# Performance work log

Measured on AMD Instinct MI355X. Metric: run time of the kernel, lower is better.

## Reference

```python
import jax, jax.numpy as jnp
import numpy as np

PATCH = 8
NP_H = 1024 // PATCH  # 128
NP_W = 1024 // PATCH  # 128
HID = (8, 8, 8)
IN_DIM = 2


def setup_inputs() -> dict:
    key = jax.random.key(0)
    ks = jax.random.split(key, 5)
    light_direction = jax.random.normal(ks[0], (32, IN_DIM), dtype=jnp.float32)
    w1 = jax.random.normal(ks[1], (NP_H, NP_W, HID[0], IN_DIM), dtype=jnp.float32) * 0.01
    b1 = jnp.zeros((NP_H, NP_W, HID[0]), dtype=jnp.float32)
    w2 = jax.random.normal(ks[2], (NP_H, NP_W, HID[1], HID[0]), dtype=jnp.float32) * 0.01
    b2 = jnp.zeros((NP_H, NP_W, HID[1]), dtype=jnp.float32)
    w3 = jax.random.normal(ks[3], (NP_H, NP_W, HID[2], HID[1]), dtype=jnp.float32) * 0.01
    b3 = jnp.zeros((NP_H, NP_W, HID[2]), dtype=jnp.float32)
    w_out = jax.random.normal(ks[4], (NP_H, NP_W, 3, HID[2]), dtype=jnp.float32) * 0.01
    b_out = jnp.zeros((NP_H, NP_W, 3), dtype=jnp.float32)
    return {"light_direction": light_direction, "w1": w1, "b1": b1,
            "w2": w2, "b2": b2, "w3": w3, "b3": b3,
            "w_out": w_out, "b_out": b_out}


def reference(light_direction, w1, b1, w2, b2, w3, b3, w_out, b_out):
    B = light_direction.shape[0]
    # broadcast light dir to every patch: [B, H, W, in_dim]
    x = jnp.broadcast_to(light_direction[:, None, None, :], (B, NP_H, NP_W, IN_DIM))
    # per-patch tiny MLP: einsum over input dim (batched tiny GEMV per patch)
    h = jax.nn.relu(jnp.einsum('bhwi,hwoi->bhwo', x, w1) + b1)
    h = jax.nn.relu(jnp.einsum('bhwi,hwoi->bhwo', h, w2) + b2)
    h = jax.nn.relu(jnp.einsum('bhwi,hwoi->bhwo', h, w3) + b3)
    out = jax.nn.sigmoid(jnp.einsum('bhwi,hwoi->bhwo', h, w_out) + b_out)  # [B,H,W,3]
    # tile each patch value to patch_size x patch_size pixels -> [B,1024,1024,3]
    out = jnp.broadcast_to(out[:, :, None, :, None, :],
                           (B, NP_H, PATCH, NP_W, PATCH, 3))
    return out.reshape(B, NP_H * PATCH, NP_W * PATCH, 3)
```

## Files before the change

### kernel.cpp

```cpp
#include <hip/hip_runtime.h>
#include <math.h>

#define NP 128
#define NB 32

typedef float vf4 __attribute__((ext_vector_type(4)));

__global__ __launch_bounds__(256) void fused_relight(
    const float* __restrict__ ld,
    const float* __restrict__ w1,
    const float* __restrict__ b1,
    const float* __restrict__ w2,
    const float* __restrict__ b2,
    const float* __restrict__ w3,
    const float* __restrict__ b3,
    const float* __restrict__ wo,
    const float* __restrict__ bo,
    float* __restrict__ out)
{
    int bid = blockIdx.x;
    int ph = bid >> 5;
    int b  = bid & 31;
    int t  = threadIdx.x;

    __shared__ float cl[NP * 3];

    if (t < NP) {
        int p = ph * NP + t;
        float x0 = ld[2 * b + 0];
        float x1 = ld[2 * b + 1];

        float h[8], g[8];
        {
            const float* W  = w1 + (size_t)p * 16;
            const float* Bv = b1 + (size_t)p * 8;
#pragma unroll
            for (int o = 0; o < 8; ++o) {
                float s = fmaf(W[2 * o + 0], x0, fmaf(W[2 * o + 1], x1, Bv[o]));
                h[o] = fmaxf(0.f, s);
            }
        }
        {
            const float* W  = w2 + (size_t)p * 64;
            const float* Bv = b2 + (size_t)p * 8;
#pragma unroll
            for (int o = 0; o < 8; ++o) {
                float s = Bv[o];
#pragma unroll
                for (int i = 0; i < 8; ++i) s = fmaf(W[8 * o + i], h[i], s);
                g[o] = fmaxf(0.f, s);
            }
        }
        {
            const float* W  = w3 + (size_t)p * 64;
            const float* Bv = b3 + (size_t)p * 8;
#pragma unroll
            for (int o = 0; o < 8; ++o) {
                float s = Bv[o];
#pragma unroll
                for (int i = 0; i < 8; ++i) s = fmaf(W[8 * o + i], g[i], s);
                h[o] = fmaxf(0.f, s);
            }
        }
        {
            const float* W  = wo + (size_t)p * 24;
            const float* Bv = bo + (size_t)p * 3;
#pragma unroll
            for (int c = 0; c < 3; ++c) {
                float s = Bv[c];
#pragma unroll
                for (int i = 0; i < 8; ++i) s = fmaf(W[8 * c + i], h[i], s);
                cl[t * 3 + c] = 1.f / (1.f + expf(-s));
            }
        }
    }
    __syncthreads();

    vf4* op = (vf4*)out + (size_t)b * 786432 + (size_t)ph * 6144;

#pragma unroll
    for (int k = 0; k < 24; ++k) {
        int c  = k * 256 + t;
        int row = c / 768;
        int ct = c - row * 768;
        int pw = ct / 6;
        int s  = ct % 3;

        float c0 = cl[pw * 3 + 0];
        float c1 = cl[pw * 3 + 1];
        float c2 = cl[pw * 3 + 2];
        float ca = (s == 0) ? c0 : ((s == 1) ? c1 : c2);
        float cb = (s == 0) ? c1 : ((s == 1) ? c2 : c0);
        float cc = (s == 0) ? c2 : ((s == 1) ? c0 : c1);

        vf4 v;
        v.x = ca; v.y = cb; v.z = cc; v.w = ca;
        __builtin_nontemporal_store(v, &op[c]);
    }
}

extern "C" void kernel_launch(void* const* d_in, const int* in_sizes, int n_in,
                              void* d_out, int out_size, void* d_ws, size_t ws_size,
                              hipStream_t stream) {
    const float* ld = (const float*)d_in[0];
    const float* w1 = (const float*)d_in[1];
    const float* b1 = (const float*)d_in[2];
    const float* w2 = (const float*)d_in[3];
    const float* b2 = (const float*)d_in[4];
    const float* w3 = (const float*)d_in[5];
    const float* b3 = (const float*)d_in[6];
    const float* wo = (const float*)d_in[7];
    const float* bo = (const float*)d_in[8];

    float* out = (float*)d_out;

    fused_relight<<<dim3(NP * NB), dim3(256), 0, stream>>>(
        ld, w1, b1, w2, b2, w3, b3, wo, bo, out);
}
```

Before: 95.79 us.

## Split fused kernel into full-occupancy MLP pass and separate tile-write pass

Splits the work into two kernels. The first runs the per-patch MLP on every thread and writes colors to a workspace buffer. The second loads those colors into shared memory and does the broadcast tile writes. This removes the idle half-block during MLP compute and the serialization of compute before stores within each block, at the cost of an extra launch and a round trip of about 6 MB through the workspace. The old fused kernel remains as a fallback when the workspace is too small.

```diff
diff --git a/kernel.cpp b/kernel.cpp
--- a/kernel.cpp
+++ b/kernel.cpp
@@ -6,7 +6,7 @@
 
 typedef float vf4 __attribute__((ext_vector_type(4)));
 
-__global__ __launch_bounds__(256) void fused_relight(
+__global__ __launch_bounds__(256) void mlp_colors(
     const float* __restrict__ ld,
     const float* __restrict__ w1,
     const float* __restrict__ b1,
@@ -16,67 +16,76 @@
     const float* __restrict__ b3,
     const float* __restrict__ wo,
     const float* __restrict__ bo,
+    float* __restrict__ color)
+{
+    unsigned int tid = blockIdx.x * blockDim.x + threadIdx.x;
+    int p = tid & 16383;
+    int b = tid >> 14;
+
+    float x0 = ld[2 * b + 0];
+    float x1 = ld[2 * b + 1];
+
+    float h[8], g[8];
+    {
+        const float* W  = w1 + (size_t)p * 16;
+        const float* Bv = b1 + (size_t)p * 8;
+#pragma unroll
+        for (int o = 0; o < 8; ++o) {
+            float s = fmaf(W[2 * o + 0], x0, fmaf(W[2 * o + 1], x1, Bv[o]));
+            h[o] = fmaxf(0.f, s);
+        }
+    }
+    {
+        const float* W  = w2 + (size_t)p * 64;
+        const float* Bv = b2 + (size_t)p * 8;
+#pragma unroll
+        for (int o = 0; o < 8; ++o) {
+            float s = Bv[o];
+#pragma unroll
+            for (int i = 0; i < 8; ++i) s = fmaf(W[8 * o + i], h[i], s);
+            g[o] = fmaxf(0.f, s);
+        }
+    }
+    {
+        const float* W  = w3 + (size_t)p * 64;
+        const float* Bv = b3 + (size_t)p * 8;
+#pragma unroll
+        for (int o = 0; o < 8; ++o) {
+            float s = Bv[o];
+#pragma unroll
+            for (int i = 0; i < 8; ++i) s = fmaf(W[8 * o + i], g[i], s);
+            h[o] = fmaxf(0.f, s);
+        }
+    }
+    {
+        const float* W  = wo + (size_t)p * 24;
+        const float* Bv = bo + (size_t)p * 3;
+        float* cp = color + ((size_t)b * 16384 + (size_t)p) * 3;
+#pragma unroll
+        for (int c = 0; c < 3; ++c) {
+            float s = Bv[c];
+#pragma unroll
+            for (int i = 0; i < 8; ++i) s = fmaf(W[8 * c + i], h[i], s);
+            cp[c] = 1.f / (1.f + expf(-s));
+        }
+    }
+}
+
+__global__ __launch_bounds__(256) void tile_write_f32(
+    const float* __restrict__ color,
     float* __restrict__ out)
 {
     int bid = blockIdx.x;
-    int ph = bid >> 5;
-    int b  = bid & 31;
-    int t  = threadIdx.x;
+    int t = threadIdx.x;
 
     __shared__ float cl[NP * 3];
 
-    if (t < NP) {
-        int p = ph * NP + t;
-        float x0 = ld[2 * b + 0];
-        float x1 = ld[2 * b + 1];
-
-        float h[8], g[8];
-        {
-            const float* W  = w1 + (size_t)p * 16;
-            const float* Bv = b1 + (size_t)p * 8;
-#pragma unroll
-            for (int o = 0; o < 8; ++o) {
-                float s = fmaf(W[2 * o + 0], x0, fmaf(W[2 * o + 1], x1, Bv[o]));
-                h[o] = fmaxf(0.f, s);
-            }
-        }
-        {
-            const float* W  = w2 + (size_t)p * 64;
-            const float* Bv = b2 + (size_t)p * 8;
-#pragma unroll
-            for (int o = 0; o < 8; ++o) {
-                float s = Bv[o];
-#pragma unroll
-                for (int i = 0; i < 8; ++i) s = fmaf(W[8 * o + i], h[i], s);
-                g[o] = fmaxf(0.f, s);
-            }
-        }
-        {
-            const float* W  = w3 + (size_t)p * 64;
-            const float* Bv = b3 + (size_t)p * 8;
-#pragma unroll
-            for (int o = 0; o < 8; ++o) {
-                float s = Bv[o];
-#pragma unroll
-                for (int i = 0; i < 8; ++i) s = fmaf(W[8 * o + i], g[i], s);
-                h[o] = fmaxf(0.f, s);
-            }
-        }
-        {
-            const float* W  = wo + (size_t)p * 24;
-            const float* Bv = bo + (size_t)p * 3;
-#pragma unroll
-            for (int c = 0; c < 3; ++c) {
-                float s = Bv[c];
-#pragma unroll
-                for (int i = 0; i < 8; ++i) s = fmaf(W[8 * c + i], h[i], s);
-                cl[t * 3 + c] = 1.f / (1.f + expf(-s));
-            }
-        }
-    }
+    const float* src = color + (size_t)bid * (NP * 3);
+    cl[t] = src[t >= 384 ? 0 : t];
+    if (t < 128) cl[256 + t] = src[256 + t];
     __syncthreads();
 
-    vf4* op = (vf4*)out + (size_t)b * 786432 + (size_t)ph * 6144;
+    vf4* op = (vf4*)out + (size_t)bid * 6144;
 
 #pragma unroll
     for (int k = 0; k < 24; ++k) {
@@ -95,6 +104,87 @@
 
         vf4 v;
         v.x = ca; v.y = cb; v.z = cc; v.w = ca;
+        __builtin_nontemporal_store(v, &op[c]);
+    }
+}
+
+__global__ __launch_bounds__(256) void fused_relight(
+    const float* __restrict__ ld, const float* __restrict__ w1,
+    const float* __restrict__ b1, const float* __restrict__ w2,
+    const float* __restrict__ b2, const float* __restrict__ w3,
+    const float* __restrict__ b3, const float* __restrict__ wo,
+    const float* __restrict__ bo, float* __restrict__ out)
+{
+    int bid = blockIdx.x;
+    int ph = bid >> 5;
+    int b  = bid & 31;
+    int t  = threadIdx.x;
+
+    __shared__ float cl[NP * 3];
+
+    if (t < NP) {
+        int p = ph * NP + t;
+        float x0 = ld[2 * b + 0];
+        float x1 = ld[2 * b + 1];
+        float h[8], g[8];
+        {
+            const float* W  = w1 + (size_t)p * 16;
+            const float* Bv = b1 + (size_t)p * 8;
+#pragma unroll
+            for (int o = 0; o < 8; ++o)
+                h[o] = fmaxf(0.f, fmaf(W[2*o], x0, fmaf(W[2*o+1], x1, Bv[o])));
+        }
+        {
+            const float* W  = w2 + (size_t)p * 64;
+            const float* Bv = b2 + (size_t)p * 8;
+#pragma unroll
+            for (int o = 0; o < 8; ++o) {
+                float s = Bv[o];
+#pragma unroll
+                for (int i = 0; i < 8; ++i) s = fmaf(W[8*o+i], h[i], s);
+                g[o] = fmaxf(0.f, s);
+            }
+        }
+        {
+            const float* W  = w3 + (size_t)p * 64;
+            const float* Bv = b3 + (size_t)p * 8;
+#pragma unroll
+            for (int o = 0; o < 8; ++o) {
+                float s = Bv[o];
+#pragma unroll
+                for (int i = 0; i < 8; ++i) s = fmaf(W[8*o+i], g[i], s);
+                h[o] = fmaxf(0.f, s);
+            }
+        }
+        {
+            const float* W  = wo + (size_t)p * 24;
+            const float* Bv = bo + (size_t)p * 3;
+#pragma unroll
+            for (int c = 0; c < 3; ++c) {
+                float s = Bv[c];
+#pragma unroll
+                for (int i = 0; i < 8; ++i) s = fmaf(W[8*c+i], h[i], s);
+                cl[t * 3 + c] = 1.f / (1.f + expf(-s));
+            }
+        }
+    }
+    __syncthreads();
+
+    vf4* op = (vf4*)out + (size_t)b * 786432 + (size_t)ph * 6144;
+#pragma unroll
+    for (int k = 0; k < 24; ++k) {
+        int c  = k * 256 + t;
+        int row = c / 768;
+        int ct = c - row * 768;
+        int pw = ct / 6;
+        int s  = ct % 3;
+        float c0 = cl[pw * 3 + 0];
+        float c1 = cl[pw * 3 + 1];
+        float c2 = cl[pw * 3 + 2];
+        float ca = (s == 0) ? c0 : ((s == 1) ? c1 : c2);
+        float cb = (s == 0) ? c1 : ((s == 1) ? c2 : c0);
+        float cc = (s == 0) ? c2 : ((s == 1) ? c0 : c1);
+        vf4 v; v.x = ca; v.y = cb; v.z = cc; v.w = ca;
         __builtin_nontemporal_store(v, &op[c]);
     }
 }
@@ -113,7 +203,15 @@
     const float* bo = (const float*)d_in[8];
 
     float* out = (float*)d_out;
-
-    fused_relight<<<dim3(NP * NB), dim3(256), 0, stream>>>(
-        ld, w1, b1, w2, b2, w3, b3, wo, bo, out);
-}
+    const size_t color_bytes = (size_t)NB * NP * NP * 3 * sizeof(float);
+
+    if (ws_size >= color_bytes) {
+        float* color = (float*)d_ws;
+        mlp_colors<<<dim3((NB * NP * NP) / 256), dim3(256), 0, stream>>>(
+            ld, w1, b1, w2, b2, w3, b3, wo, bo, color);
+        tile_write_f32<<<dim3(NB * NP), dim3(256), 0, stream>>>(color, out);
+    } else {
+        fused_relight<<<dim3(NP * NB), dim3(256), 0, stream>>>(
+            ld, w1, b1, w2, b2, w3, b3, wo, bo, out);
+    }
+}
```

Result: slower. 128.2 us (+33.9%).
